# Performance work log

Hardware: AMD Instinct MI355X
Metric: run time of the kernel (lower is better)

## Reference

```python
import jax, jax.numpy as jnp
import numpy as np

D_MODEL = 1024
D_STATE = 16
BATCH = 4
SEQLEN = 4096


def setup_inputs() -> dict:
    key = jax.random.key(0)
    kx, kA, kB, kC = jax.random.split(key, 4)
    x = jax.random.normal(kx, (BATCH, SEQLEN, D_MODEL), dtype=jnp.float32)
    # Params per init_weights(): A ~ N(-0.5, 0.1), B ~ N(0, 0.1), C ~ N(0, 0.1), D = 0
    A = -0.5 + 0.1 * jax.random.normal(kA, (1, D_STATE), dtype=jnp.float32)
    B_in = 0.1 * jax.random.normal(kB, (D_MODEL, D_STATE), dtype=jnp.float32)
    C = 0.1 * jax.random.normal(kC, (D_STATE, D_MODEL), dtype=jnp.float32)
    D = jnp.zeros((D_MODEL,), dtype=jnp.float32)
    return {"x": x, "A": A, "B_in": B_in, "C": C, "D": D}


def reference(x, A, B_in, C, D):
    # x: [B, N, E]; A: [1, S]; B_in: [E, S]; C: [S, E]; D: [E]
    A_neg = -jnp.exp(A)                              # [1, S]
    Bx = jnp.einsum('bne,es->bns', x, B_in)          # [B, N, S] = x @ B
    delta = jax.nn.softplus(Bx)                      # softplus(u @ B)
    decay = jnp.exp(delta * A_neg)                   # [B, N, S]

    def step(h, inp):
        d_t, bx_t = inp                              # each [B, S]
        h = h * d_t + bx_t
        return h, h

    h0 = jnp.zeros((x.shape[0], A.shape[1]), dtype=x.dtype)
    # scan over time: inputs [N, B, S]
    _, hs = jax.lax.scan(step, h0, (decay.transpose(1, 0, 2), Bx.transpose(1, 0, 2)))
    # readout: y_t = h_t @ C + x_t * D  (dropout p=0.0 -> identity)
    y = jnp.einsum('nbs,se->bne', hs, C) + x * D
    return y
```

## Files before the change

kernel.cpp:

```cpp
#include <hip/hip_runtime.h>

#define NSEQ 4096
#define EDIM 1024

__device__ float  g_pbx[4 * 64 * NSEQ];
__device__ float2 g_hp [64 * NSEQ];
__device__ float2 g_sum[64 * 16];

__device__ __forceinline__ void fma4(float4& a, float xv, const float4& b) {
    a.x = fmaf(xv, b.x, a.x);
    a.y = fmaf(xv, b.y, a.y);
    a.z = fmaf(xv, b.z, a.z);
    a.w = fmaf(xv, b.w, a.w);
}

__global__ __launch_bounds__(256, 4) void k1_bx(const float* __restrict__ x,
                                                const float* __restrict__ Bin) {
    __shared__ float red[4 * 64 * 17];
    const int tid  = threadIdx.x;
    const int lane = tid & 63;
    const int wu   = __builtin_amdgcn_readfirstlane(tid) >> 6;
    const int q    = blockIdx.x & 3;
    const int r0   = (blockIdx.x >> 2) * 64;
    const int b    = r0 >> 12;
    const int n0   = r0 & 4095;
    const int eq   = q * 256;

    const float4* xf4 = (const float4*)x;
    const float4* Bf4 = (const float4*)Bin;

    float4 xr[16];
    const size_t rowb = (size_t)(r0 + lane) * 256 + q * 64 + wu * 4;
#pragma unroll
    for (int c = 0; c < 4; c++)
#pragma unroll
        for (int jj = 0; jj < 4; jj++)
            xr[c * 4 + jj] = xf4[rowb + c * 16 + jj];

    float acc[16];
#pragma unroll
    for (int s = 0; s < 16; s++) acc[s] = 0.f;

#pragma unroll
    for (int c = 0; c < 4; ++c) {
#pragma unroll
        for (int jj = 0; jj < 4; ++jj) {
            const float4 xq = xr[c * 4 + jj];
            const float xs[4] = {xq.x, xq.y, xq.z, xq.w};
#pragma unroll
            for (int m = 0; m < 4; ++m) {
                const int e = eq + c * 64 + wu * 16 + jj * 4 + m;
                const float4 b0 = Bf4[e * 4 + 0];
                const float4 b1 = Bf4[e * 4 + 1];
                const float4 b2 = Bf4[e * 4 + 2];
                const float4 b3 = Bf4[e * 4 + 3];
                const float xv = xs[m];
                acc[0]  = fmaf(xv, b0.x, acc[0]);  acc[1]  = fmaf(xv, b0.y, acc[1]);
                acc[2]  = fmaf(xv, b0.z, acc[2]);  acc[3]  = fmaf(xv, b0.w, acc[3]);
                acc[4]  = fmaf(xv, b1.x, acc[4]);  acc[5]  = fmaf(xv, b1.y, acc[5]);
                acc[6]  = fmaf(xv, b1.z, acc[6]);  acc[7]  = fmaf(xv, b1.w, acc[7]);
                acc[8]  = fmaf(xv, b2.x, acc[8]);  acc[9]  = fmaf(xv, b2.y, acc[9]);
                acc[10] = fmaf(xv, b2.z, acc[10]); acc[11] = fmaf(xv, b2.w, acc[11]);
                acc[12] = fmaf(xv, b3.x, acc[12]); acc[13] = fmaf(xv, b3.y, acc[13]);
                acc[14] = fmaf(xv, b3.z, acc[14]); acc[15] = fmaf(xv, b3.w, acc[15]);
            }
        }
    }

    {
        const int rb = (wu * 64 + lane) * 17;
#pragma unroll
        for (int s = 0; s < 16; s++) red[rb + s] = acc[s];
    }
    __syncthreads();

#pragma unroll
    for (int p = 0; p < 4; p++) {
        const int o   = tid + 256 * p;
        const int s   = o >> 6;
        const int row = o & 63;
        const float v = red[(0 * 64 + row) * 17 + s] + red[(1 * 64 + row) * 17 + s] +
                        red[(2 * 64 + row) * 17 + s] + red[(3 * 64 + row) * 17 + s];
        g_pbx[(size_t)q * 262144u + (size_t)(b * 16 + s) * NSEQ + n0 + row] = v;
    }
}

__global__ __launch_bounds__(256) void k2_scan(const float* __restrict__ A) {
    __shared__ float sP[4], sH[4];
    const int tid   = threadIdx.x;
    const int lane  = tid & 63;
    const int w     = tid >> 6;
    const int chain = blockIdx.x >> 4;
    const int chunk = blockIdx.x & 15;
    const int ss    = chain & 15;
    const int t     = chunk * 256 + tid;

    float bxv = 0.f;
#pragma unroll
    for (int q = 0; q < 4; q++)
        bxv += g_pbx[(size_t)q * 262144u + (size_t)chain * NSEQ + t];

    const float Ae = expf(A[ss]);
    const float sp = fmaxf(bxv, 0.f) + log1pf(expf(-fabsf(bxv)));
    const float de = expf(-Ae * sp);

    float Pi = de, hi = bxv;
#pragma unroll
    for (int off = 1; off < 64; off <<= 1) {
        float Pp = __shfl_up(Pi, off, 64);
        float hp = __shfl_up(hi, off, 64);
        if (lane >= off) { hi = fmaf(hp, Pi, hi); Pi *= Pp; }
    }
    if (lane == 63) { sP[w] = Pi; sH[w] = hi; }
    __syncthreads();
    float Hw = 0.f, Pw = 1.f;
    for (int qq = 0; qq < w; qq++) { Hw = fmaf(Hw, sP[qq], sH[qq]); Pw *= sP[qq]; }

    const float hloc = fmaf(Hw, Pi, hi);
    const float pinc = Pw * Pi;
    g_hp[(size_t)chain * NSEQ + t] = make_float2(hloc, pinc);
    if (tid == 255)
        g_sum[chain * 16 + chunk] = make_float2(hloc, pinc);
}

__global__ __launch_bounds__(256) void k3_out(const float* __restrict__ x,
                                              const float* __restrict__ C,
                                              const float* __restrict__ D,
                                              float* __restrict__ out) {
    __shared__ __align__(16) float sh[16 * 20];
    const int tid = threadIdx.x;
    const int blk = blockIdx.x;
    const int tc  = blk & 255;
    const int b   = blk >> 8;
    const int t0  = tc * 16;

    {
        const int s  = tid >> 4;
        const int tt = tid & 15;
        const int chain = b * 16 + s;
        const int t = t0 + tt;
        const int chunk = t >> 8;
        float H = 0.f;
        for (int c = 0; c < chunk; ++c) {
            const float2 su = g_sum[chain * 16 + c];
            H = fmaf(H, su.y, su.x);
        }
        const float2 hp = g_hp[(size_t)chain * NSEQ + t];
        sh[tt * 20 + s] = fmaf(hp.y, H, hp.x);
    }

    const float4* C4 = (const float4*)C;
    float4 creg[16];
#pragma unroll
    for (int s = 0; s < 16; s++) creg[s] = C4[s * 256 + tid];
    const float4 dreg = ((const float4*)D)[tid];
    const bool needX = __any((dreg.x != 0.f) | (dreg.y != 0.f) |
                             (dreg.z != 0.f) | (dreg.w != 0.f));
    __syncthreads();

    const float4* x4 = (const float4*)x;
    float4* o4 = (float4*)out;
    const size_t rowbase = ((size_t)b * NSEQ + t0) * 256;

    if (needX) {
#pragma unroll 4
        for (int tt = 0; tt < 16; tt++) {
            float4 xv = x4[rowbase + tt * 256 + tid];
            float4 y;
            y.x = xv.x * dreg.x; y.y = xv.y * dreg.y;
            y.z = xv.z * dreg.z; y.w = xv.w * dreg.w;
#pragma unroll
            for (int g = 0; g < 4; g++) {
                const float4 h4 = *(const float4*)&sh[tt * 20 + g * 4];
                fma4(y, h4.x, creg[g * 4 + 0]);
                fma4(y, h4.y, creg[g * 4 + 1]);
                fma4(y, h4.z, creg[g * 4 + 2]);
                fma4(y, h4.w, creg[g * 4 + 3]);
            }
            o4[rowbase + tt * 256 + tid] = y;
        }
    } else {
#pragma unroll 4
        for (int tt = 0; tt < 16; tt++) {
            float4 y = make_float4(0.f, 0.f, 0.f, 0.f);
#pragma unroll
            for (int g = 0; g < 4; g++) {
                const float4 h4 = *(const float4*)&sh[tt * 20 + g * 4];
                fma4(y, h4.x, creg[g * 4 + 0]);
                fma4(y, h4.y, creg[g * 4 + 1]);
                fma4(y, h4.z, creg[g * 4 + 2]);
                fma4(y, h4.w, creg[g * 4 + 3]);
            }
            o4[rowbase + tt * 256 + tid] = y;
        }
    }
}

extern "C" void kernel_launch(void* const* d_in, const int* in_sizes, int n_in,
                              void* d_out, int out_size, void* d_ws, size_t ws_size,
                              hipStream_t stream) {
    const float* x   = (const float*)d_in[0];
    const float* A   = (const float*)d_in[1];
    const float* Bin = (const float*)d_in[2];
    const float* C   = (const float*)d_in[3];
    const float* D   = (const float*)d_in[4];
    float* out = (float*)d_out;
    (void)d_ws; (void)ws_size;

    hipLaunchKernelGGL(k1_bx,   dim3(1024), dim3(256), 0, stream, x, Bin);
    hipLaunchKernelGGL(k2_scan, dim3(1024), dim3(256), 0, stream, A);
    hipLaunchKernelGGL(k3_out,  dim3(1024), dim3(256), 0, stream, x, C, D, out);
}
```

Before: 135.3 us.

## Stage x tiles through per-wave LDS double buffer with coalesced loads in k1

Rewrites the x loads in the Bx projection kernel. Each group of four lanes now reads one row segment, so loads are more contiguous. The tiles are written into a per-wave LDS double buffer and read back per lane, and the next chunk is prefetched while the current one is computed. The aim is better global load coalescing and overlap of memory latency with FMAs. It costs extra LDS traffic and LDS space, and it issues float4 LDS accesses at 17-float row strides that are not 16-byte aligned.

```diff
diff --git a/kernel.cpp b/kernel.cpp
--- a/kernel.cpp
+++ b/kernel.cpp
@@ -16,7 +16,7 @@
 
 __global__ __launch_bounds__(256, 4) void k1_bx(const float* __restrict__ x,
                                                 const float* __restrict__ Bin) {
-    __shared__ float red[4 * 64 * 17];
+    __shared__ __align__(16) float smem[4 * 2 * 64 * 17];
     const int tid  = threadIdx.x;
     const int lane = tid & 63;
     const int wu   = __builtin_amdgcn_readfirstlane(tid) >> 6;
@@ -29,48 +29,63 @@
     const float4* xf4 = (const float4*)x;
     const float4* Bf4 = (const float4*)Bin;
 
-    float4 xr[16];
-    const size_t rowb = (size_t)(r0 + lane) * 256 + q * 64 + wu * 4;
-#pragma unroll
-    for (int c = 0; c < 4; c++)
-#pragma unroll
-        for (int jj = 0; jj < 4; jj++)
-            xr[c * 4 + jj] = xf4[rowb + c * 16 + jj];
+    const int wbase = wu * 2176;
+    const int srow  = lane >> 2;
+    const int sc4   = lane & 3;
+
+    float4 pf[4];
+#pragma unroll
+    for (int k = 0; k < 4; k++)
+        pf[k] = xf4[(size_t)(r0 + srow + 16 * k) * 256 + q * 64 + wu * 4 + sc4];
+#pragma unroll
+    for (int k = 0; k < 4; k++)
+        *(float4*)&smem[wbase + (srow + 16 * k) * 17 + sc4 * 4] = pf[k];
 
     float acc[16];
 #pragma unroll
     for (int s = 0; s < 16; s++) acc[s] = 0.f;
 
-#pragma unroll
     for (int c = 0; c < 4; ++c) {
-#pragma unroll
-        for (int jj = 0; jj < 4; ++jj) {
-            const float4 xq = xr[c * 4 + jj];
-            const float xs[4] = {xq.x, xq.y, xq.z, xq.w};
-#pragma unroll
-            for (int m = 0; m < 4; ++m) {
-                const int e = eq + c * 64 + wu * 16 + jj * 4 + m;
-                const float4 b0 = Bf4[e * 4 + 0];
-                const float4 b1 = Bf4[e * 4 + 1];
-                const float4 b2 = Bf4[e * 4 + 2];
-                const float4 b3 = Bf4[e * 4 + 3];
-                const float xv = xs[m];
-                acc[0]  = fmaf(xv, b0.x, acc[0]);  acc[1]  = fmaf(xv, b0.y, acc[1]);
-                acc[2]  = fmaf(xv, b0.z, acc[2]);  acc[3]  = fmaf(xv, b0.w, acc[3]);
-                acc[4]  = fmaf(xv, b1.x, acc[4]);  acc[5]  = fmaf(xv, b1.y, acc[5]);
-                acc[6]  = fmaf(xv, b1.z, acc[6]);  acc[7]  = fmaf(xv, b1.w, acc[7]);
-                acc[8]  = fmaf(xv, b2.x, acc[8]);  acc[9]  = fmaf(xv, b2.y, acc[9]);
-                acc[10] = fmaf(xv, b2.z, acc[10]); acc[11] = fmaf(xv, b2.w, acc[11]);
-                acc[12] = fmaf(xv, b3.x, acc[12]); acc[13] = fmaf(xv, b3.y, acc[13]);
-                acc[14] = fmaf(xv, b3.z, acc[14]); acc[15] = fmaf(xv, b3.w, acc[15]);
-            }
+        if (c < 3) {
+#pragma unroll
+            for (int k = 0; k < 4; k++)
+                pf[k] = xf4[(size_t)(r0 + srow + 16 * k) * 256 + q * 64 +
+                            (c + 1) * 16 + wu * 4 + sc4];
+        }
+        __builtin_amdgcn_sched_barrier(0);
+
+        const float* buf = &smem[wbase + (c & 1) * 1088];
+#pragma unroll
+        for (int el = 0; el < 16; ++el) {
+            const float xv = buf[lane * 17 + el];
+            const int e = eq + c * 64 + wu * 16 + el;
+            const float4 b0 = Bf4[e * 4 + 0];
+            const float4 b1 = Bf4[e * 4 + 1];
+            const float4 b2 = Bf4[e * 4 + 2];
+            const float4 b3 = Bf4[e * 4 + 3];
+            acc[0]  = fmaf(xv, b0.x, acc[0]);  acc[1]  = fmaf(xv, b0.y, acc[1]);
+            acc[2]  = fmaf(xv, b0.z, acc[2]);  acc[3]  = fmaf(xv, b0.w, acc[3]);
+            acc[4]  = fmaf(xv, b1.x, acc[4]);  acc[5]  = fmaf(xv, b1.y, acc[5]);
+            acc[6]  = fmaf(xv, b1.z, acc[6]);  acc[7]  = fmaf(xv, b1.w, acc[7]);
+            acc[8]  = fmaf(xv, b2.x, acc[8]);  acc[9]  = fmaf(xv, b2.y, acc[9]);
+            acc[10] = fmaf(xv, b2.z, acc[10]); acc[11] = fmaf(xv, b2.w, acc[11]);
+            acc[12] = fmaf(xv, b3.x, acc[12]); acc[13] = fmaf(xv, b3.y, acc[13]);
+            acc[14] = fmaf(xv, b3.z, acc[14]); acc[15] = fmaf(xv, b3.w, acc[15]);
+        }
+
+        __builtin_amdgcn_sched_barrier(0);
+        if (c < 3) {
+            float* dst = &smem[wbase + ((c + 1) & 1) * 1088];
+#pragma unroll
+            for (int k = 0; k < 4; k++)
+                *(float4*)&dst[(srow + 16 * k) * 17 + sc4 * 4] = pf[k];
         }
     }
 
     {
-        const int rb = (wu * 64 + lane) * 17;
-#pragma unroll
-        for (int s = 0; s < 16; s++) red[rb + s] = acc[s];
+        const int rb = wbase + lane * 17;
+#pragma unroll
+        for (int s = 0; s < 16; s++) smem[rb + s] = acc[s];
     }
     __syncthreads();
 
@@ -79,8 +94,8 @@
         const int o   = tid + 256 * p;
         const int s   = o >> 6;
         const int row = o & 63;
-        const float v = red[(0 * 64 + row) * 17 + s] + red[(1 * 64 + row) * 17 + s] +
-                        red[(2 * 64 + row) * 17 + s] + red[(3 * 64 + row) * 17 + s];
+        const float v = smem[0 * 2176 + row * 17 + s] + smem[1 * 2176 + row * 17 + s] +
+                        smem[2 * 2176 + row * 17 + s] + smem[3 * 2176 + row * 17 + s];
         g_pbx[(size_t)q * 262144u + (size_t)(b * 16 + s) * NSEQ + n0 + row] = v;
     }
 }
```

After: 151.5 us. 1.12x slower.
